# Kernel tuning notes

Hardware: AMD Instinct MI355X
Metric: run time of the kernel (lower is better)

Reference implementation:

```python
import jax, jax.numpy as jnp
import numpy as np

D_MODEL = 1024
HEADS = 16


def setup_inputs() -> dict:
    key = jax.random.key(0)
    ks = jax.random.split(key, 5)
    S = 4096
    x = jax.random.normal(ks[0], (S, D_MODEL), dtype=jnp.float32)
    scale = 1.0 / np.sqrt(D_MODEL)
    Wq = jax.random.normal(ks[1], (D_MODEL, D_MODEL), dtype=jnp.float32) * scale
    Wk = jax.random.normal(ks[2], (D_MODEL, D_MODEL), dtype=jnp.float32) * scale
    Wv = jax.random.normal(ks[3], (D_MODEL, D_MODEL), dtype=jnp.float32) * scale
    Wo = jax.random.normal(ks[4], (D_MODEL, D_MODEL), dtype=jnp.float32) * scale
    return {"x": x, "Wq": Wq, "Wk": Wk, "Wv": Wv, "Wo": Wo}


def reference(x, Wq, Wk, Wv, Wo):
    # x: [S, D]; weights follow torch Linear convention y = x @ W.T
    S, D = x.shape
    H = HEADS
    d_k = D // H
    q = (x @ Wq.T).reshape(S, H, d_k)  # [S,H,dk]
    k = (x @ Wk.T).reshape(S, H, d_k)
    v = (x @ Wv.T).reshape(S, H, d_k)
    # logits: [H, S, S] = q k^T / sqrt(d_k)
    logits = jnp.einsum('shd,thd->hst', q, k) / jnp.sqrt(jnp.asarray(d_k, x.dtype))
    probs = jax.nn.softmax(logits, axis=-1)
    out = jnp.einsum('hst,thd->shd', probs, v).reshape(S, D)
    return out @ Wo.T
```

## Files before the change

kernel.cpp:

```cpp
#include <hip/hip_runtime.h>
#include <hip/hip_bf16.h>


typedef __bf16 bf16_t;
typedef __bf16 bf16x8 __attribute__((ext_vector_type(8)));
typedef __bf16 bf16x4 __attribute__((ext_vector_type(4)));
typedef float f32x4 __attribute__((ext_vector_type(4)));

#define D_MODEL 1024
#define SEQ 4096
#define HEADS 16
#define DK 64
#define QSCALE 0.1803368801111204f
#define EXP2_MAGIC 8404859.0f

__global__ void cast_all(const float* __restrict__ x, const float* __restrict__ a,
                         const float* __restrict__ b, const float* __restrict__ c,
                         const float* __restrict__ d, bf16_t* __restrict__ xb,
                         bf16_t* __restrict__ wb) {
    const int gi = blockIdx.x * blockDim.x + threadIdx.x;
    const float* src; bf16_t* dst; int i;
    if (gi < SEQ * D_MODEL / 4) {
        src = x; dst = xb; i = gi * 4;
    } else {
        int g = gi - SEQ * D_MODEL / 4;
        int which = g >> 18;
        src = which == 0 ? a : which == 1 ? b : which == 2 ? c : d;
        dst = wb + (size_t)which * D_MODEL * D_MODEL;
        i = (g & 0x3FFFF) * 4;
    }
    float4 v = *(const float4*)(src + i);
    bf16x4 o;
    o[0] = (bf16_t)v.x; o[1] = (bf16_t)v.y; o[2] = (bf16_t)v.z; o[3] = (bf16_t)v.w;
    *(bf16x4*)(dst + i) = o;
}

__device__ __forceinline__ void g2l16(const bf16_t* g, bf16_t* l) {
    __builtin_amdgcn_global_load_lds(
        (const __attribute__((address_space(1))) void*)g,
        (__attribute__((address_space(3))) void*)l, 16, 0, 0);
}

__device__ __forceinline__ bf16x8 exp2_pk(const f32x4 a, const f32x4 b) {
    union { float f; unsigned u; } v[8];
#pragma unroll
    for (int r = 0; r < 4; r++) {
        v[r].f     = fmaf(a[r], 128.0f, EXP2_MAGIC);
        v[r + 4].f = fmaf(b[r], 128.0f, EXP2_MAGIC);
    }
    union { unsigned u[4]; bf16x8 h; } o;
#pragma unroll
    for (int p = 0; p < 4; p++)
        o.u[p] = __builtin_amdgcn_perm(v[2 * p + 1].u, v[2 * p].u, 0x05040100u);
    return o.h;
}

template <int ROUTE>
__global__ __launch_bounds__(256, 2) void gemm_lds(const bf16_t* __restrict__ A,
                                                   const bf16_t* __restrict__ B,
                                                   void* __restrict__ out0,
                                                   void* __restrict__ out1,
                                                   void* __restrict__ out2,
                                                   int M, int N, int K) {
    __shared__ __align__(16) bf16_t As[2][128 * 64];
    __shared__ __align__(16) bf16_t Bs[2][128 * 64];

    const int tid = threadIdx.x;
    const int lane = tid & 63;
    const int wave = tid >> 6;
    const int l15 = lane & 15;
    const int lg  = lane >> 4;

    const int flat = blockIdx.y * gridDim.x + blockIdx.x;
    const int mpx  = gridDim.y >> 3;
    const int xcd  = flat & 7;
    const int pos  = flat >> 3;
    const int m0 = (xcd * mpx + (pos % mpx)) * 128;
    const int n0 = (pos / mpx) * 128;
    const int wm = (wave >> 1) * 64;
    const int wn = (wave & 1) * 64;

    const bf16_t* aSrc[4]; const bf16_t* bSrc[4];
    int sOff[4];
#pragma unroll
    for (int it = 0; it < 4; it++) {
        int c = it * 256 + tid;
        int row = c >> 3, cc = (c & 7) ^ (row & 7);
        aSrc[it] = A + (size_t)(m0 + row) * K + cc * 8;
        bSrc[it] = B + (size_t)(n0 + row) * K + cc * 8;
        sOff[it] = c * 8;
    }

    int aoff[2][4], boff[2][4];
#pragma unroll
    for (int kk = 0; kk < 2; kk++) {
#pragma unroll
        for (int i = 0; i < 4; i++) {
            int row = wm + i * 16 + l15;
            aoff[kk][i] = row * 64 + (((kk << 2) | lg) ^ (row & 7)) * 8;
        }
#pragma unroll
        for (int j = 0; j < 4; j++) {
            int row = wn + j * 16 + l15;
            boff[kk][j] = row * 64 + (((kk << 2) | lg) ^ (row & 7)) * 8;
        }
    }

    f32x4 acc[4][4];
#pragma unroll
    for (int i = 0; i < 4; i++)
#pragma unroll
        for (int j = 0; j < 4; j++) acc[i][j] = f32x4{0.f, 0.f, 0.f, 0.f};

#pragma unroll
    for (int it = 0; it < 4; it++) g2l16(aSrc[it], &As[0][sOff[it]]);
#pragma unroll
    for (int it = 0; it < 4; it++) g2l16(bSrc[it], &Bs[0][sOff[it]]);

    const int nsteps = K / 64;
    for (int s = 0; s < nsteps; s++) {
        const int cur = s & 1;
        __syncthreads();

        if (s + 1 < nsteps) {
            const int nxt = cur ^ 1;
            const int k1 = (s + 1) * 64;
#pragma unroll
            for (int it = 0; it < 4; it++) g2l16(aSrc[it] + k1, &As[nxt][sOff[it]]);
#pragma unroll
            for (int it = 0; it < 4; it++) g2l16(bSrc[it] + k1, &Bs[nxt][sOff[it]]);
        }

        const bf16_t* Ab_ = As[cur];
        const bf16_t* Bb_ = Bs[cur];
#pragma unroll
        for (int kk = 0; kk < 2; kk++) {
            bf16x8 af[4], bfm[4];
#pragma unroll
            for (int i = 0; i < 4; i++) af[i] = *(const bf16x8*)(Ab_ + aoff[kk][i]);
#pragma unroll
            for (int j = 0; j < 4; j++) bfm[j] = *(const bf16x8*)(Bb_ + boff[kk][j]);
#pragma unroll
            for (int i = 0; i < 4; i++)
#pragma unroll
                for (int j = 0; j < 4; j++)
                    acc[i][j] = __builtin_amdgcn_mfma_f32_16x16x32_bf16(af[i], bfm[j], acc[i][j], 0, 0, 0);
        }
    }

    const int ng = n0 + wn;
    if (ROUTE == 0) {
        float* C = (float*)out0;
#pragma unroll
        for (int i = 0; i < 4; i++)
#pragma unroll
            for (int r = 0; r < 4; r++) {
                int m = m0 + wm + i * 16 + lg * 4 + r;
                float* crow = C + (size_t)m * N + ng;
#pragma unroll
                for (int j = 0; j < 4; j++) crow[j * 16 + l15] = acc[i][j][r];
            }
    } else {
        if (ng < 2048) {
            const bool isQ = (ng < 1024);
            const float sc = isQ ? QSCALE : 1.0f;
            bf16_t* dst = isQ ? (bf16_t*)out0 : (bf16_t*)out1;
            int nn = ng & 1023;
#pragma unroll
            for (int i = 0; i < 4; i++)
#pragma unroll
                for (int r = 0; r < 4; r++) {
                    int m = m0 + wm + i * 16 + lg * 4 + r;
                    bf16_t* crow = dst + (size_t)m * D_MODEL + nn;
#pragma unroll
                    for (int j = 0; j < 4; j++) crow[j * 16 + l15] = (bf16_t)(acc[i][j][r] * sc);
                }
        } else {
            bf16_t* Vt = (bf16_t*)out2;
#pragma unroll
            for (int i = 0; i < 4; i++)
#pragma unroll
                for (int j = 0; j < 4; j++) {
                    int vcol = ng - 2048 + j * 16 + l15;
                    int m = m0 + wm + i * 16 + lg * 4;
                    int mp = (m & ~31) | (((m >> 2) & 3) << 3) | (((m >> 4) & 1) << 2);
                    bf16x4 v4;
#pragma unroll
                    for (int r = 0; r < 4; r++) v4[r] = (bf16_t)acc[i][j][r];
                    *(bf16x4*)(Vt + (size_t)vcol * SEQ + mp) = v4;
                }
        }
    }
}

__global__ __launch_bounds__(512, 2) void attn_kernel(const bf16_t* __restrict__ Q,
                                                      const bf16_t* __restrict__ Km,
                                                      const bf16_t* __restrict__ Vt,
                                                      bf16_t* __restrict__ O) {
    const int tid = threadIdx.x;
    const int lane = tid & 63;
    const int wave = tid >> 6;
    const int l15 = lane & 15;
    const int lg  = lane >> 4;
    const int bid = blockIdx.x;
    const int h    = (bid & 7) * 2 + ((bid >> 3) & 1);
    const int qblk = bid >> 4;
    const int q0 = qblk * 256;
    const int hoff = h * DK;

    __shared__ struct {
        __align__(16) bf16_t K[2][64 * 64];
        __align__(16) bf16_t V[2][64 * 64];
    } sm;

    bf16x8 qf[2][2];
#pragma unroll
    for (int t = 0; t < 2; t++)
#pragma unroll
        for (int c = 0; c < 2; c++)
            qf[t][c] = *(const bf16x8*)(Q + (size_t)(q0 + wave * 32 + t * 16 + l15) * D_MODEL
                                        + hoff + c * 32 + lg * 8);

    f32x4 oacc[2][4], lfrag[2];
#pragma unroll
    for (int t = 0; t < 2; t++) {
        lfrag[t] = f32x4{0.f, 0.f, 0.f, 0.f};
#pragma unroll
        for (int dt = 0; dt < 4; dt++) oacc[t][dt] = f32x4{0.f, 0.f, 0.f, 0.f};
    }

    bf16x8 ones8;
#pragma unroll
    for (int j = 0; j < 8; j++) ones8[j] = (bf16_t)1.0f;

    const int srow = tid >> 3;
    const int sdc = (tid & 7) ^ (srow & 7);
    const bf16_t* kSrc = Km + (size_t)srow * D_MODEL + hoff + sdc * 8;
    const bf16_t* vSrc = Vt + (size_t)(hoff + srow) * SEQ + sdc * 8;

    int kOff[4][2], vOff[2][4];
#pragma unroll
    for (int kt = 0; kt < 4; kt++)
#pragma unroll
        for (int c = 0; c < 2; c++) {
            int row = kt * 16 + l15;
            kOff[kt][c] = row * 64 + (((c * 4 + lg) ^ (row & 7)) * 8);
        }
#pragma unroll
    for (int kp = 0; kp < 2; kp++)
#pragma unroll
        for (int dt = 0; dt < 4; dt++) {
            int row = dt * 16 + l15;
            vOff[kp][dt] = row * 64 + (((kp * 4 + lg) ^ (row & 7)) * 8);
        }

    g2l16(kSrc, &sm.K[0][tid * 8]);
    g2l16(vSrc, &sm.V[0][tid * 8]);

    for (int s = 0; s < SEQ / 64; s++) {
        const int cur = s & 1;
        __syncthreads();

        if (s + 1 < SEQ / 64) {
            const int nxt = cur ^ 1;
            g2l16(kSrc + (size_t)(s + 1) * 64 * D_MODEL, &sm.K[nxt][tid * 8]);
            g2l16(vSrc + (s + 1) * 64,                   &sm.V[nxt][tid * 8]);
        }

        const bf16_t* Kb = sm.K[cur];
        const bf16_t* Vb = sm.V[cur];

#pragma unroll
        for (int kp = 0; kp < 2; kp++) {
            bf16x8 vf[4];
#pragma unroll
            for (int dt = 0; dt < 4; dt++) vf[dt] = *(const bf16x8*)(Vb + vOff[kp][dt]);

            f32x4 st[2][2];
#pragma unroll
            for (int sub = 0; sub < 2; sub++) {
                const int kt = kp * 2 + sub;
                const bf16x8 kf0 = *(const bf16x8*)(Kb + kOff[kt][0]);
                const bf16x8 kf1 = *(const bf16x8*)(Kb + kOff[kt][1]);
#pragma unroll
                for (int t = 0; t < 2; t++) {
                    f32x4 a = f32x4{0.f, 0.f, 0.f, 0.f};
                    a = __builtin_amdgcn_mfma_f32_16x16x32_bf16(kf0, qf[t][0], a, 0, 0, 0);
                    a = __builtin_amdgcn_mfma_f32_16x16x32_bf16(kf1, qf[t][1], a, 0, 0, 0);
                    st[t][sub] = a;
                }
            }

#pragma unroll
            for (int t = 0; t < 2; t++) {
                const bf16x8 pbig = exp2_pk(st[t][0], st[t][1]);
                lfrag[t] = __builtin_amdgcn_mfma_f32_16x16x32_bf16(ones8, pbig, lfrag[t], 0, 0, 0);
#pragma unroll
                for (int dt = 0; dt < 4; dt++)
                    oacc[t][dt] = __builtin_amdgcn_mfma_f32_16x16x32_bf16(vf[dt], pbig, oacc[t][dt], 0, 0, 0);
            }
        }
    }

#pragma unroll
    for (int t = 0; t < 2; t++) {
        const float inv = 1.f / lfrag[t][0];
        const size_t qrow = (size_t)(q0 + wave * 32 + t * 16 + l15);
#pragma unroll
        for (int dt = 0; dt < 4; dt++) {
            bf16x4 o4;
#pragma unroll
            for (int r = 0; r < 4; r++) o4[r] = (bf16_t)(oacc[t][dt][r] * inv);
            *(bf16x4*)(O + qrow * D_MODEL + hoff + dt * 16 + lg * 4) = o4;
        }
    }
}

extern "C" void kernel_launch(void* const* d_in, const int* in_sizes, int n_in,
                              void* d_out, int out_size, void* d_ws, size_t ws_size,
                              hipStream_t stream) {
    const float* x  = (const float*)d_in[0];
    const float* Wq = (const float*)d_in[1];
    const float* Wk = (const float*)d_in[2];
    const float* Wv = (const float*)d_in[3];
    const float* Wo = (const float*)d_in[4];
    float* out = (float*)d_out;

    char* ws = (char*)d_ws;
    bf16_t* xb  = (bf16_t*)(ws);
    bf16_t* wqb = (bf16_t*)(ws + (8u  << 20));
    bf16_t* wob = (bf16_t*)(ws + (14u << 20));
    bf16_t* Qb  = (bf16_t*)(ws + (16u << 20));
    bf16_t* Kb  = (bf16_t*)(ws + (24u << 20));
    bf16_t* Vtb = (bf16_t*)(ws + (32u << 20));
    bf16_t* Ab  = (bf16_t*)(ws + (40u << 20));

    cast_all<<<8192, 256, 0, stream>>>(x, Wq, Wk, Wv, Wo, xb, wqb);

    gemm_lds<1><<<dim3(3 * D_MODEL / 128, SEQ / 128), 256, 0, stream>>>(
        xb, wqb, Qb, Kb, Vtb, SEQ, 3 * D_MODEL, D_MODEL);

    attn_kernel<<<256, 512, 0, stream>>>(Qb, Kb, Vtb, Ab);

    gemm_lds<0><<<dim3(D_MODEL / 128, SEQ / 128), 256, 0, stream>>>(
        Ab, wob, out, nullptr, nullptr, SEQ, D_MODEL, D_MODEL);
}
```

Baseline: 195.6 us.

## Restructure GEMM main loop into explicit two-stage pipeline with partial vmcnt waits

Replaces the double-buffered loop, which issued a full __syncthreads each step, with an unrolled two-buffer ping-pong. Each step waits with s_waitcnt vmcnt(8), so only the older stage's global-to-LDS loads must finish while the next stage's loads stay in flight. Raw s_barrier and sched_barrier calls pin the instruction order. Loads wrap around with a mask past the last K tile, which issues redundant loads at the end and assumes nsteps is an even power of two.

```diff
diff --git a/kernel.cpp b/kernel.cpp
--- a/kernel.cpp
+++ b/kernel.cpp
@@ -62,8 +62,10 @@
                                                    void* __restrict__ out1,
                                                    void* __restrict__ out2,
                                                    int M, int N, int K) {
-    __shared__ __align__(16) bf16_t As[2][128 * 64];
-    __shared__ __align__(16) bf16_t Bs[2][128 * 64];
+    __shared__ __align__(16) bf16_t As0[128 * 64];
+    __shared__ __align__(16) bf16_t As1[128 * 64];
+    __shared__ __align__(16) bf16_t Bs0[128 * 64];
+    __shared__ __align__(16) bf16_t Bs1[128 * 64];
 
     const int tid = threadIdx.x;
     const int lane = tid & 63;
@@ -112,27 +114,14 @@
 #pragma unroll
         for (int j = 0; j < 4; j++) acc[i][j] = f32x4{0.f, 0.f, 0.f, 0.f};
 
-#pragma unroll
-    for (int it = 0; it < 4; it++) g2l16(aSrc[it], &As[0][sOff[it]]);
-#pragma unroll
-    for (int it = 0; it < 4; it++) g2l16(bSrc[it], &Bs[0][sOff[it]]);
-
-    const int nsteps = K / 64;
-    for (int s = 0; s < nsteps; s++) {
-        const int cur = s & 1;
-        __syncthreads();
-
-        if (s + 1 < nsteps) {
-            const int nxt = cur ^ 1;
-            const int k1 = (s + 1) * 64;
-#pragma unroll
-            for (int it = 0; it < 4; it++) g2l16(aSrc[it] + k1, &As[nxt][sOff[it]]);
-#pragma unroll
-            for (int it = 0; it < 4; it++) g2l16(bSrc[it] + k1, &Bs[nxt][sOff[it]]);
-        }
-
-        const bf16_t* Ab_ = As[cur];
-        const bf16_t* Bb_ = Bs[cur];
+    auto STAGE = [&](int kt, bf16_t* Ad, bf16_t* Bd) {
+        const int k0 = kt * 64;
+#pragma unroll
+        for (int it = 0; it < 4; it++) g2l16(aSrc[it] + k0, Ad + sOff[it]);
+#pragma unroll
+        for (int it = 0; it < 4; it++) g2l16(bSrc[it] + k0, Bd + sOff[it]);
+    };
+    auto COMPUTE = [&](const bf16_t* Ab_, const bf16_t* Bb_) {
 #pragma unroll
         for (int kk = 0; kk < 2; kk++) {
             bf16x8 af[4], bfm[4];
@@ -146,6 +135,28 @@
                 for (int j = 0; j < 4; j++)
                     acc[i][j] = __builtin_amdgcn_mfma_f32_16x16x32_bf16(af[i], bfm[j], acc[i][j], 0, 0, 0);
         }
+    };
+
+    const int nsteps = K / 64;
+    STAGE(0, As0, Bs0);
+    STAGE(1, As1, Bs1);
+
+    for (int s = 0; s < nsteps; s += 2) {
+        asm volatile("s_waitcnt vmcnt(8)" ::: "memory");
+        __builtin_amdgcn_s_barrier();
+        __builtin_amdgcn_sched_barrier(0);
+        COMPUTE(As0, Bs0);
+        __builtin_amdgcn_s_barrier();
+        __builtin_amdgcn_sched_barrier(0);
+        STAGE((s + 2) & (nsteps - 1), As0, Bs0);
+
+        asm volatile("s_waitcnt vmcnt(8)" ::: "memory");
+        __builtin_amdgcn_s_barrier();
+        __builtin_amdgcn_sched_barrier(0);
+        COMPUTE(As1, Bs1);
+        __builtin_amdgcn_s_barrier();
+        __builtin_amdgcn_sched_barrier(0);
+        STAGE((s + 3) & (nsteps - 1), As1, Bs1);
     }
 
     const int ng = n0 + wn;
```

After: 187.6 us. -4.1%, faster.
